# Kernel optimization log

Hardware: AMD Instinct MI355X
Metric: run time of the kernel (lower is better)

Reference implementation:

```python
import jax, jax.numpy as jnp
import numpy as np

K = 128
T_X = 4
DATA_LENGTH = 512
B_GROUPS = 64
B = B_GROUPS * DATA_LENGTH
INV_SQRT2 = 0.7071067811865476  # 1/sqrt(2), haar reconstruction filter coeff


def setup_inputs() -> dict:
    key = jax.random.key(0)
    ks = jax.random.split(key, 9)
    x = jax.random.normal(ks[0], (B, T_X, K), jnp.float32)
    y = jax.random.normal(ks[1], (B, 1, K), jnp.float32)
    s = 1.0 / np.sqrt(K).astype(np.float32)
    Wq = jax.random.normal(ks[2], (K, K), jnp.float32) * s
    Wk = jax.random.normal(ks[3], (K, K), jnp.float32) * s
    Wv = jax.random.normal(ks[4], (K, K), jnp.float32) * s
    conv_w = jax.random.normal(ks[5], (K, 2 * K), jnp.float32) * (1.0 / np.sqrt(2 * K).astype(np.float32))
    conv_b = jax.random.normal(ks[6], (K,), jnp.float32) * 0.01
    bn_gamma = jnp.ones((K,), jnp.float32)
    bn_beta = jnp.zeros((K,), jnp.float32)
    bn_mean = jax.random.normal(ks[7], (K,), jnp.float32) * 0.1
    bn_var = jax.random.uniform(ks[8], (K,), jnp.float32, 0.5, 1.5)
    return dict(x=x, y=y, Wq=Wq, Wk=Wk, Wv=Wv, conv_w=conv_w, conv_b=conv_b,
                bn_gamma=bn_gamma, bn_beta=bn_beta, bn_mean=bn_mean, bn_var=bn_var,
                data_length=DATA_LENGTH)


def _idwt_haar(L, H):
    # inverse 1D haar transform along last dim: (Bg, C, 1, T) -> (Bg, C, 1, 2T)
    even = (L + H) * INV_SQRT2
    odd = (L - H) * INV_SQRT2
    out = jnp.stack([even, odd], axis=-1)  # (..., T, 2)
    return out.reshape(L.shape[:-1] + (L.shape[-1] * 2,))


def reference(x, y, Wq, Wk, Wv, conv_w, conv_b, bn_gamma, bn_beta, bn_mean, bn_var, data_length):
    b, t_x, k = x.shape  # t_x = 4 bands, heads = 1, t_y = 1
    q = jnp.einsum('btk,ok->bto', y, Wq)                      # (b, 1, k)
    keys = jnp.einsum('bsk,ok->bso', x, Wk) * (1.0 / (k ** 0.5))  # (b, 4, k)
    v = jnp.einsum('bsk,ok->bso', x, Wv)                      # (b, 4, k)
    dot = jnp.einsum('bto,bso->bs', q, keys)                  # (b, 4)
    w = jax.nn.softmax(dot, axis=1)                           # softmax over the 4 bands
    outs = w[:, :, None] * v                                  # (b, 4, k) band-weighted values
    Bg = b // data_length
    # per band: (b, k) -> (Bg, dl, 1, k) -> permute -> (Bg, k, 1, dl)
    o = outs.reshape(Bg, data_length, t_x, k).transpose(2, 0, 3, 1)  # (4, Bg, k, dl)
    o = o[:, :, :, None, :]                                   # (4, Bg, k, 1, dl)
    out_L = _idwt_haar(o[0], o[1])                            # (Bg, k, 1, 2*dl)
    out_H = _idwt_haar(o[2], o[3])
    out = jnp.concatenate([out_L, out_H], axis=1)             # (Bg, 2k, 1, 2*dl)
    # transition: 1x1 conv + BN (eval mode) + LeakyReLU(0.01)
    z = jnp.einsum('bcij,oc->boij', out, conv_w) + conv_b[None, :, None, None]
    scale = (bn_gamma * jax.lax.rsqrt(bn_var + 1e-5))[None, :, None, None]
    z = (z - bn_mean[None, :, None, None]) * scale + bn_beta[None, :, None, None]
    return jnp.where(z > 0, z, 0.01 * z)
```

## Files before the change

### kernel.cpp

```cpp
#include <hip/hip_runtime.h>
#include <stdint.h>

typedef __attribute__((ext_vector_type(8))) short bf16x8;
typedef __attribute__((ext_vector_type(4))) float f32x4;

__device__ __forceinline__ unsigned short f2bf(float x) {
    union { float f; uint32_t u; } v; v.f = x;
    uint32_t r = v.u + 0x7FFFu + ((v.u >> 16) & 1u);
    return (unsigned short)(r >> 16);
}
__device__ __forceinline__ uint32_t pack2bf(float a, float b) {
    return (uint32_t)f2bf(a) | ((uint32_t)f2bf(b) << 16);
}
__device__ __forceinline__ float bf2f(uint32_t lo) {
    union { uint32_t u; float f; } v; v.u = lo << 16; return v.f;
}
__device__ __forceinline__ float lrelu(float v) { return v > 0.f ? v : 0.01f * v; }

__global__ __launch_bounds__(256) void precompute_kernel(
    const float* __restrict__ Wq, const float* __restrict__ Wk,
    const float* __restrict__ Wv, const float* __restrict__ conv_w,
    const float* __restrict__ conv_b, const float* __restrict__ bn_gamma,
    const float* __restrict__ bn_beta, const float* __restrict__ bn_mean,
    const float* __restrict__ bn_var,
    unsigned short* __restrict__ Gh, unsigned short* __restrict__ Gl,
    unsigned short* __restrict__ Mh, unsigned short* __restrict__ Ml,
    float* __restrict__ scale2, float* __restrict__ bias2)
{
    if (blockIdx.x == 384) {
        int o = threadIdx.x;
        if (o < 128) {
            float sc = bn_gamma[o] * rsqrtf(bn_var[o] + 1e-5f);
            scale2[o] = sc;
            bias2[o]  = (conv_b[o] - bn_mean[o]) * sc + bn_beta[o];
        }
        return;
    }
    int gid  = blockIdx.x * 256 + threadIdx.x;
    int oi   = gid >> 1;
    int half = gid & 1;
    float sum = 0.f;
    if (oi < 16384) {
        int i = oi >> 7, j = oi & 127;
        const float* wk = Wk + half * 64 * 128 + i;
        const float* wq = Wq + half * 64 * 128 + j;
        #pragma unroll 8
        for (int o = 0; o < 64; ++o) sum += wk[o * 128] * wq[o * 128];
        sum += __shfl_xor(sum, 1);
        if (!half) {
            float val = sum * 0.08838834764831845f;
            unsigned short h = f2bf(val);
            Gh[i * 128 + j] = h;
            Gl[i * 128 + j] = f2bf(val - bf2f(h));
        }
    } else {
        int rel = oi - 16384;
        int o = rel >> 8, c = rel & 255;
        const float* cw = conv_w + o * 256 + ((c >> 7) << 7) + half * 64;
        const float* wv = Wv + half * 64 * 128 + (c & 127);
        #pragma unroll 8
        for (int t = 0; t < 64; ++t) sum += cw[t] * wv[t * 128];
        sum += __shfl_xor(sum, 1);
        if (!half) {
            float val = sum * 0.7071067811865476f;
            unsigned short h = f2bf(val);
            Mh[o * 256 + c] = h;
            Ml[o * 256 + c] = f2bf(val - bf2f(h));
        }
    }
}

#define UADDR(row, lane) (((row) << 8) + (((((lane) >> 2) ^ ((row) & 7))) << 4) + ((((lane) << 2)) & 15))
#define AADDR(row, gi)   (((row) << 8) + ((((gi) ^ ((row) & 7))) << 4))

__global__ __launch_bounds__(256) void fused_kernel(
    const float* __restrict__ x, const float* __restrict__ y,
    const unsigned short* __restrict__ Gh, const unsigned short* __restrict__ Gl,
    const unsigned short* __restrict__ Mh, const unsigned short* __restrict__ Ml,
    const float* __restrict__ scale2, const float* __restrict__ bias2,
    float* __restrict__ out)
{
    __shared__ __align__(16) unsigned char smem[65536];
    float* gbufF = (float*)(smem + 32768);

    const int tid = threadIdx.x;
    const int w = tid >> 6;
    const int l = tid & 63;
    const int quad = l >> 4;
    const int bid = blockIdx.x;
    const int b0 = bid * 64;

    {
        const float* yb = y + (size_t)b0 * 128;
        #pragma unroll
        for (int it = 0; it < 8; ++it) {
            int idx = tid + it * 256;
            int row = idx >> 5, q = idx & 31;
            float4 v = *(const float4*)(yb + row * 128 + q * 4);
            *(float4*)(smem + row * 512 + ((q ^ (row & 7)) << 4)) = v;
        }
    }
    __syncthreads();

    {
        f32x4 accg[8];
        #pragma unroll
        for (int nt = 0; nt < 8; ++nt) accg[nt] = (f32x4){0.f, 0.f, 0.f, 0.f};
        const int yrow = 16 * w + (l & 15);
        #pragma unroll
        for (int ks = 0; ks < 4; ++ks) {
            int g0 = ks * 8 + quad * 2;
            float4 v0 = *(const float4*)(smem + yrow * 512 + (((g0 + 0) ^ (yrow & 7)) << 4));
            float4 v1 = *(const float4*)(smem + yrow * 512 + (((g0 + 1) ^ (yrow & 7)) << 4));
            float f[8] = {v0.x, v0.y, v0.z, v0.w, v1.x, v1.y, v1.z, v1.w};
            union { bf16x8 v; unsigned short u[8]; } Ah, Al;
            #pragma unroll
            for (int j = 0; j < 8; ++j) {
                unsigned short h = f2bf(f[j]);
                Ah.u[j] = h;
                Al.u[j] = f2bf(f[j] - bf2f(h));
            }
            #pragma unroll
            for (int nt = 0; nt < 8; ++nt) {
                int off = (nt * 16 + (l & 15)) * 128 + ks * 32 + quad * 8;
                bf16x8 bh = *(const bf16x8*)(Gh + off);
                bf16x8 bl = *(const bf16x8*)(Gl + off);
                accg[nt] = __builtin_amdgcn_mfma_f32_16x16x32_bf16(Ah.v, bh, accg[nt], 0, 0, 0);
                accg[nt] = __builtin_amdgcn_mfma_f32_16x16x32_bf16(Al.v, bh, accg[nt], 0, 0, 0);
                accg[nt] = __builtin_amdgcn_mfma_f32_16x16x32_bf16(Ah.v, bl, accg[nt], 0, 0, 0);
            }
        }
        #pragma unroll
        for (int nt = 0; nt < 8; ++nt) {
            int i = nt * 16 + (l & 15);
            #pragma unroll
            for (int r = 0; r < 4; ++r) {
                int srow = 16 * w + quad * 4 + r;
                gbufF[srow * 128 + i] = accg[nt][r];
            }
        }
    }

    #pragma unroll 4
    for (int s = 0; s < 16; ++s) {
        int b_loc = w * 16 + s;
        const float2* xb = (const float2*)(x + (size_t)(b0 + b_loc) * 512);
        float2 x0 = xb[l], x1 = xb[64 + l], x2 = xb[128 + l], x3 = xb[192 + l];
        float2 g2 = *(const float2*)(gbufF + b_loc * 128 + 2 * l);
        float p0 = x0.x * g2.x + x0.y * g2.y;
        float p1 = x1.x * g2.x + x1.y * g2.y;
        float p2 = x2.x * g2.x + x2.y * g2.y;
        float p3 = x3.x * g2.x + x3.y * g2.y;
        #pragma unroll
        for (int off = 32; off >= 1; off >>= 1) {
            p0 += __shfl_xor(p0, off);
            p1 += __shfl_xor(p1, off);
            p2 += __shfl_xor(p2, off);
            p3 += __shfl_xor(p3, off);
        }
        float mx = fmaxf(fmaxf(p0, p1), fmaxf(p2, p3));
        float e0 = __expf(p0 - mx), e1 = __expf(p1 - mx);
        float e2 = __expf(p2 - mx), e3 = __expf(p3 - mx);
        float inv = 1.f / (e0 + e1 + e2 + e3);
        float w0 = e0 * inv, w1 = e1 * inv, w2 = e2 * inv, w3 = e3 * inv;
        int r0 = 2 * b_loc, r1 = r0 + 1;
        *(uint32_t*)(smem + UADDR(r0, l)) = pack2bf(w0 * x0.x + w1 * x1.x, w0 * x0.y + w1 * x1.y);
        *(uint32_t*)(smem + UADDR(r1, l)) = pack2bf(w0 * x0.x - w1 * x1.x, w0 * x0.y - w1 * x1.y);
        *(uint32_t*)(smem + 32768 + UADDR(r0, l)) = pack2bf(w2 * x2.x + w3 * x3.x, w2 * x2.y + w3 * x3.y);
        *(uint32_t*)(smem + 32768 + UADDR(r1, l)) = pack2bf(w2 * x2.x - w3 * x3.x, w2 * x2.y - w3 * x3.y);
    }

    f32x4 acc[2][8];
    #pragma unroll
    for (int m = 0; m < 2; ++m)
        #pragma unroll
        for (int nt = 0; nt < 8; ++nt) acc[m][nt] = (f32x4){0.f, 0.f, 0.f, 0.f};

    #pragma unroll
    for (int ks = 0; ks < 8; ++ks) {
        int half = ks >> 2, kk = ks & 3;
        int base = half << 15;
        int row0 = 32 * w + (l & 15);
        int row1 = row0 + 16;
        int gi = kk * 4 + quad;
        bf16x8 a0 = *(const bf16x8*)(smem + base + AADDR(row0, gi));
        bf16x8 a1 = *(const bf16x8*)(smem + base + AADDR(row1, gi));
        #pragma unroll
        for (int nt = 0; nt < 8; ++nt) {
            int off = (nt * 16 + (l & 15)) * 256 + half * 128 + kk * 32 + quad * 8;
            bf16x8 bh = *(const bf16x8*)(Mh + off);
            bf16x8 bl = *(const bf16x8*)(Ml + off);
            acc[0][nt] = __builtin_amdgcn_mfma_f32_16x16x32_bf16(a0, bh, acc[0][nt], 0, 0, 0);
            acc[0][nt] = __builtin_amdgcn_mfma_f32_16x16x32_bf16(a0, bl, acc[0][nt], 0, 0, 0);
            acc[1][nt] = __builtin_amdgcn_mfma_f32_16x16x32_bf16(a1, bh, acc[1][nt], 0, 0, 0);
            acc[1][nt] = __builtin_amdgcn_mfma_f32_16x16x32_bf16(a1, bl, acc[1][nt], 0, 0, 0);
        }
    }

    {
        int out_g = bid >> 3;
        int j0 = (bid & 7) * 128;
        float* outp = out + (size_t)out_g * 131072 + j0;
        #pragma unroll
        for (int nt = 0; nt < 8; ++nt) {
            int o = nt * 16 + (l & 15);
            float sc = scale2[o], bi = bias2[o];
            #pragma unroll
            for (int m = 0; m < 2; ++m) {
                int jb = (2 * w + m) * 16 + quad * 4;
                f32x4 a = acc[m][nt];
                float4 r;
                r.x = lrelu(a[0] * sc + bi);
                r.y = lrelu(a[1] * sc + bi);
                r.z = lrelu(a[2] * sc + bi);
                r.w = lrelu(a[3] * sc + bi);
                *(float4*)(outp + (size_t)o * 1024 + jb) = r;
            }
        }
    }
}

extern "C" void kernel_launch(void* const* d_in, const int* in_sizes, int n_in,
                              void* d_out, int out_size, void* d_ws, size_t ws_size,
                              hipStream_t stream)
{
    (void)in_sizes; (void)n_in; (void)out_size; (void)ws_size;
    const float* x        = (const float*)d_in[0];
    const float* y        = (const float*)d_in[1];
    const float* Wq       = (const float*)d_in[2];
    const float* Wk       = (const float*)d_in[3];
    const float* Wv       = (const float*)d_in[4];
    const float* conv_w   = (const float*)d_in[5];
    const float* conv_b   = (const float*)d_in[6];
    const float* bn_gamma = (const float*)d_in[7];
    const float* bn_beta  = (const float*)d_in[8];
    const float* bn_mean  = (const float*)d_in[9];
    const float* bn_var   = (const float*)d_in[10];

    unsigned char* ws = (unsigned char*)d_ws;
    unsigned short* Gh = (unsigned short*)(ws);
    unsigned short* Gl = (unsigned short*)(ws + 32768);
    unsigned short* Mh = (unsigned short*)(ws + 65536);
    unsigned short* Ml = (unsigned short*)(ws + 131072);
    float* scale2      = (float*)(ws + 196608);
    float* bias2       = (float*)(ws + 197120);

    hipLaunchKernelGGL(precompute_kernel, dim3(385), dim3(256), 0, stream,
                       Wq, Wk, Wv, conv_w, conv_b, bn_gamma, bn_beta, bn_mean,
                       bn_var, Gh, Gl, Mh, Ml, scale2, bias2);
    hipLaunchKernelGGL(fused_kernel, dim3(512), dim3(256), 0, stream,
                       x, y, Gh, Gl, Mh, Ml, scale2, bias2, (float*)d_out);
}
```

Measured before the change: 182.6 us.

## Halve fused tile to 32 rows, double grid, and LDS-tile weight precompute

The fused kernel now processes 32 batch rows per block instead of 64, halving LDS use to 32KB and doubling the grid to 1024 blocks. This should raise occupancy and spread work across more CUs. The Q·K Gram GEMM is split across wave pairs by column half, and a missing barrier before the gbuf reads is added. The precompute kernel is rewritten to stage 16x16 weight tiles in padded LDS instead of making strided global reads. The trade-off is that each block now reloads the Mh/Ml and Gh/Gl weights for half as many rows, so global weight traffic rises.

```diff
diff --git a/kernel.cpp b/kernel.cpp
--- a/kernel.cpp
+++ b/kernel.cpp
@@ -27,46 +27,61 @@
     unsigned short* __restrict__ Mh, unsigned short* __restrict__ Ml,
     float* __restrict__ scale2, float* __restrict__ bias2)
 {
-    if (blockIdx.x == 384) {
-        int o = threadIdx.x;
-        if (o < 128) {
-            float sc = bn_gamma[o] * rsqrtf(bn_var[o] + 1e-5f);
-            scale2[o] = sc;
-            bias2[o]  = (conv_b[o] - bn_mean[o]) * sc + bn_beta[o];
+    __shared__ float lds0[2176];
+    __shared__ float lds1[2176];
+    const int tid = threadIdx.x;
+    const int bid = blockIdx.x;
+
+    if (bid == 192) {
+        if (tid < 128) {
+            float sc = bn_gamma[tid] * rsqrtf(bn_var[tid] + 1e-5f);
+            scale2[tid] = sc;
+            bias2[tid]  = (conv_b[tid] - bn_mean[tid]) * sc + bn_beta[tid];
         }
         return;
     }
-    int gid  = blockIdx.x * 256 + threadIdx.x;
-    int oi   = gid >> 1;
-    int half = gid & 1;
-    float sum = 0.f;
-    if (oi < 16384) {
-        int i = oi >> 7, j = oi & 127;
-        const float* wk = Wk + half * 64 * 128 + i;
-        const float* wq = Wq + half * 64 * 128 + j;
+
+    if (bid < 64) {
+        int i0 = (bid >> 3) << 4, j0 = (bid & 7) << 4;
+        #pragma unroll
+        for (int t = 0; t < 8; ++t) {
+            int e = tid + t * 256;
+            int o = e >> 4, c = e & 15;
+            lds0[o * 17 + c] = Wk[o * 128 + i0 + c];
+            lds1[o * 17 + c] = Wq[o * 128 + j0 + c];
+        }
+        __syncthreads();
+        int ti = tid >> 4, tj = tid & 15;
+        float sum = 0.f;
         #pragma unroll 8
-        for (int o = 0; o < 64; ++o) sum += wk[o * 128] * wq[o * 128];
-        sum += __shfl_xor(sum, 1);
-        if (!half) {
-            float val = sum * 0.08838834764831845f;
-            unsigned short h = f2bf(val);
-            Gh[i * 128 + j] = h;
-            Gl[i * 128 + j] = f2bf(val - bf2f(h));
-        }
+        for (int o = 0; o < 128; ++o) sum += lds0[o * 17 + ti] * lds1[o * 17 + tj];
+        float val = sum * 0.08838834764831845f;
+        unsigned short h = f2bf(val);
+        int idx = (i0 + ti) * 128 + j0 + tj;
+        Gh[idx] = h;
+        Gl[idx] = f2bf(val - bf2f(h));
     } else {
-        int rel = oi - 16384;
-        int o = rel >> 8, c = rel & 255;
-        const float* cw = conv_w + o * 256 + ((c >> 7) << 7) + half * 64;
-        const float* wv = Wv + half * 64 * 128 + (c & 127);
+        int rel = bid - 64;
+        int o0 = (rel >> 4) << 4, c0 = (rel & 15) << 4;
+        int cw0 = (c0 >> 7) << 7, cc0 = c0 & 127;
+        #pragma unroll
+        for (int t = 0; t < 8; ++t) {
+            int e = tid + t * 256;
+            int to = e >> 7, k = e & 127;
+            lds0[to * 132 + k] = conv_w[(o0 + to) * 256 + cw0 + k];
+            int kk = e >> 4, c = e & 15;
+            lds1[kk * 17 + c] = Wv[kk * 128 + cc0 + c];
+        }
+        __syncthreads();
+        int to = tid >> 4, tc = tid & 15;
+        float sum = 0.f;
         #pragma unroll 8
-        for (int t = 0; t < 64; ++t) sum += cw[t] * wv[t * 128];
-        sum += __shfl_xor(sum, 1);
-        if (!half) {
-            float val = sum * 0.7071067811865476f;
-            unsigned short h = f2bf(val);
-            Mh[o * 256 + c] = h;
-            Ml[o * 256 + c] = f2bf(val - bf2f(h));
-        }
+        for (int k = 0; k < 128; ++k) sum += lds0[to * 132 + k] * lds1[k * 17 + tc];
+        float val = sum * 0.7071067811865476f;
+        unsigned short h = f2bf(val);
+        int idx = (o0 + to) * 256 + c0 + tc;
+        Mh[idx] = h;
+        Ml[idx] = f2bf(val - bf2f(h));
     }
 }
 
@@ -80,20 +95,20 @@
     const float* __restrict__ scale2, const float* __restrict__ bias2,
     float* __restrict__ out)
 {
-    __shared__ __align__(16) unsigned char smem[65536];
-    float* gbufF = (float*)(smem + 32768);
+    __shared__ __align__(16) unsigned char smem[32768];
+    float* gbufF = (float*)(smem + 16384);
 
     const int tid = threadIdx.x;
     const int w = tid >> 6;
     const int l = tid & 63;
     const int quad = l >> 4;
     const int bid = blockIdx.x;
-    const int b0 = bid * 64;
+    const int b0 = bid * 32;
 
     {
         const float* yb = y + (size_t)b0 * 128;
         #pragma unroll
-        for (int it = 0; it < 8; ++it) {
+        for (int it = 0; it < 4; ++it) {
             int idx = tid + it * 256;
             int row = idx >> 5, q = idx & 31;
             float4 v = *(const float4*)(yb + row * 128 + q * 4);
@@ -103,10 +118,11 @@
     __syncthreads();
 
     {
-        f32x4 accg[8];
-        #pragma unroll
-        for (int nt = 0; nt < 8; ++nt) accg[nt] = (f32x4){0.f, 0.f, 0.f, 0.f};
-        const int yrow = 16 * w + (l & 15);
+        const int rw = w & 1, ch = w >> 1;
+        f32x4 accg[4];
+        #pragma unroll
+        for (int n = 0; n < 4; ++n) accg[n] = (f32x4){0.f, 0.f, 0.f, 0.f};
+        const int yrow = 16 * rw + (l & 15);
         #pragma unroll
         for (int ks = 0; ks < 4; ++ks) {
             int g0 = ks * 8 + quad * 2;
@@ -121,29 +137,29 @@
                 Al.u[j] = f2bf(f[j] - bf2f(h));
             }
             #pragma unroll
-            for (int nt = 0; nt < 8; ++nt) {
+            for (int n = 0; n < 4; ++n) {
+                int nt = ch * 4 + n;
                 int off = (nt * 16 + (l & 15)) * 128 + ks * 32 + quad * 8;
                 bf16x8 bh = *(const bf16x8*)(Gh + off);
                 bf16x8 bl = *(const bf16x8*)(Gl + off);
-                accg[nt] = __builtin_amdgcn_mfma_f32_16x16x32_bf16(Ah.v, bh, accg[nt], 0, 0, 0);
-                accg[nt] = __builtin_amdgcn_mfma_f32_16x16x32_bf16(Al.v, bh, accg[nt], 0, 0, 0);
-                accg[nt] = __builtin_amdgcn_mfma_f32_16x16x32_bf16(Ah.v, bl, accg[nt], 0, 0, 0);
+                accg[n] = __builtin_amdgcn_mfma_f32_16x16x32_bf16(Ah.v, bh, accg[n], 0, 0, 0);
+                accg[n] = __builtin_amdgcn_mfma_f32_16x16x32_bf16(Al.v, bh, accg[n], 0, 0, 0);
+                accg[n] = __builtin_amdgcn_mfma_f32_16x16x32_bf16(Ah.v, bl, accg[n], 0, 0, 0);
             }
         }
         #pragma unroll
-        for (int nt = 0; nt < 8; ++nt) {
-            int i = nt * 16 + (l & 15);
+        for (int n = 0; n < 4; ++n) {
+            int i = (ch * 4 + n) * 16 + (l & 15);
             #pragma unroll
-            for (int r = 0; r < 4; ++r) {
-                int srow = 16 * w + quad * 4 + r;
-                gbufF[srow * 128 + i] = accg[nt][r];
-            }
-        }
-    }
+            for (int r = 0; r < 4; ++r)
+                gbufF[(16 * rw + quad * 4 + r) * 128 + i] = accg[n][r];
+        }
+    }
+    __syncthreads();
 
     #pragma unroll 4
-    for (int s = 0; s < 16; ++s) {
-        int b_loc = w * 16 + s;
+    for (int s = 0; s < 8; ++s) {
+        int b_loc = 8 * w + s;
         const float2* xb = (const float2*)(x + (size_t)(b0 + b_loc) * 512);
         float2 x0 = xb[l], x1 = xb[64 + l], x2 = xb[128 + l], x3 = xb[192 + l];
         float2 g2 = *(const float2*)(gbufF + b_loc * 128 + 2 * l);
@@ -166,56 +182,45 @@
         int r0 = 2 * b_loc, r1 = r0 + 1;
         *(uint32_t*)(smem + UADDR(r0, l)) = pack2bf(w0 * x0.x + w1 * x1.x, w0 * x0.y + w1 * x1.y);
         *(uint32_t*)(smem + UADDR(r1, l)) = pack2bf(w0 * x0.x - w1 * x1.x, w0 * x0.y - w1 * x1.y);
-        *(uint32_t*)(smem + 32768 + UADDR(r0, l)) = pack2bf(w2 * x2.x + w3 * x3.x, w2 * x2.y + w3 * x3.y);
-        *(uint32_t*)(smem + 32768 + UADDR(r1, l)) = pack2bf(w2 * x2.x - w3 * x3.x, w2 * x2.y - w3 * x3.y);
-    }
-
-    f32x4 acc[2][8];
+        *(uint32_t*)(smem + 16384 + UADDR(r0, l)) = pack2bf(w2 * x2.x + w3 * x3.x, w2 * x2.y + w3 * x3.y);
+        *(uint32_t*)(smem + 16384 + UADDR(r1, l)) = pack2bf(w2 * x2.x - w3 * x3.x, w2 * x2.y - w3 * x3.y);
+    }
+
+    f32x4 acc[8];
     #pragma unroll
-    for (int m = 0; m < 2; ++m)
-        #pragma unroll
-        for (int nt = 0; nt < 8; ++nt) acc[m][nt] = (f32x4){0.f, 0.f, 0.f, 0.f};
+    for (int nt = 0; nt < 8; ++nt) acc[nt] = (f32x4){0.f, 0.f, 0.f, 0.f};
 
     #pragma unroll
     for (int ks = 0; ks < 8; ++ks) {
         int half = ks >> 2, kk = ks & 3;
-        int base = half << 15;
-        int row0 = 32 * w + (l & 15);
-        int row1 = row0 + 16;
+        int base = half << 14;
+        int row0 = 16 * w + (l & 15);
         int gi = kk * 4 + quad;
         bf16x8 a0 = *(const bf16x8*)(smem + base + AADDR(row0, gi));
-        bf16x8 a1 = *(const bf16x8*)(smem + base + AADDR(row1, gi));
         #pragma unroll
         for (int nt = 0; nt < 8; ++nt) {
             int off = (nt * 16 + (l & 15)) * 256 + half * 128 + kk * 32 + quad * 8;
             bf16x8 bh = *(const bf16x8*)(Mh + off);
             bf16x8 bl = *(const bf16x8*)(Ml + off);
-            acc[0][nt] = __builtin_amdgcn_mfma_f32_16x16x32_bf16(a0, bh, acc[0][nt], 0, 0, 0);
-            acc[0][nt] = __builtin_amdgcn_mfma_f32_16x16x32_bf16(a0, bl, acc[0][nt], 0, 0, 0);
-            acc[1][nt] = __builtin_amdgcn_mfma_f32_16x16x32_bf16(a1, bh, acc[1][nt], 0, 0, 0);
-            acc[1][nt] = __builtin_amdgcn_mfma_f32_16x16x32_bf16(a1, bl, acc[1][nt], 0, 0, 0);
+            acc[nt] = __builtin_amdgcn_mfma_f32_16x16x32_bf16(a0, bh, acc[nt], 0, 0, 0);
+            acc[nt] = __builtin_amdgcn_mfma_f32_16x16x32_bf16(a0, bl, acc[nt], 0, 0, 0);
         }
     }
 
     {
-        int out_g = bid >> 3;
-        int j0 = (bid & 7) * 128;
-        float* outp = out + (size_t)out_g * 131072 + j0;
+        float* outp = out + (size_t)(bid >> 4) * 131072 + (bid & 15) * 64;
+        int jb = 16 * w + quad * 4;
         #pragma unroll
         for (int nt = 0; nt < 8; ++nt) {
             int o = nt * 16 + (l & 15);
             float sc = scale2[o], bi = bias2[o];
-            #pragma unroll
-            for (int m = 0; m < 2; ++m) {
-                int jb = (2 * w + m) * 16 + quad * 4;
-                f32x4 a = acc[m][nt];
-                float4 r;
-                r.x = lrelu(a[0] * sc + bi);
-                r.y = lrelu(a[1] * sc + bi);
-                r.z = lrelu(a[2] * sc + bi);
-                r.w = lrelu(a[3] * sc + bi);
-                *(float4*)(outp + (size_t)o * 1024 + jb) = r;
-            }
+            f32x4 a = acc[nt];
+            float4 r;
+            r.x = lrelu(a[0] * sc + bi);
+            r.y = lrelu(a[1] * sc + bi);
+            r.z = lrelu(a[2] * sc + bi);
+            r.w = lrelu(a[3] * sc + bi);
+            *(float4*)(outp + (size_t)o * 1024 + jb) = r;
         }
     }
 }
@@ -245,9 +250,9 @@
     float* scale2      = (float*)(ws + 196608);
     float* bias2       = (float*)(ws + 197120);
 
-    hipLaunchKernelGGL(precompute_kernel, dim3(385), dim3(256), 0, stream,
+    hipLaunchKernelGGL(precompute_kernel, dim3(193), dim3(256), 0, stream,
                        Wq, Wk, Wv, conv_w, conv_b, bn_gamma, bn_beta, bn_mean,
                        bn_var, Gh, Gl, Mh, Ml, scale2, bias2);
-    hipLaunchKernelGGL(fused_kernel, dim3(512), dim3(256), 0, stream,
+    hipLaunchKernelGGL(fused_kernel, dim3(1024), dim3(256), 0, stream,
                        x, y, Gh, Gl, Mh, Ml, scale2, bias2, (float*)d_out);
 }
```

After: 199.8 us. 9.5% more time.
